# Kernel optimization log

Hardware: AMD Instinct MI355X
Metric: run time of the kernel (lower is better)

## Reference

```python
import jax, jax.numpy as jnp
import numpy as np

NE, NR, D, H, L = 200000, 500, 128, 4, 2
HD = D // H
N, E, B = 32768, 262144, 256
MARGIN = 1.0


def setup_inputs() -> dict:
    key = jax.random.key(0)
    ks = jax.random.split(key, 16)
    nrm = lambda k, shp, s=0.05: jax.random.normal(k, shp, jnp.float32) * s
    inp = {
        'ent_emb': nrm(ks[0], (NE, D)),
        'rel_emb': nrm(ks[1], (NR, D)),
        'rel_prior': nrm(ks[2], (NR, 1)),
    }
    for i, nm in enumerate(['Wq', 'Wk', 'Wv', 'Wo', 'Wek', 'Wev']):
        inp[nm] = nrm(ks[3 + i], (L, D, D))
    for gi, g in enumerate(['h', 't', 'n']):
        kb = jax.random.fold_in(key, 100 + gi)
        k1, k2, k3, k4 = jax.random.split(kb, 4)
        inp[f'x_{g}'] = jax.random.randint(k1, (N,), 0, NE, jnp.int32)
        inp[f'ei_{g}'] = jax.random.randint(k2, (2, E), 0, N, jnp.int32)
        inp[f'ea_{g}'] = jax.random.randint(k3, (E,), 0, NR, jnp.int32)
        inp[f'y_{g}'] = jax.random.randint(k4, (B,), 0, N // B, jnp.int32)
        inp[f's_{g}'] = jnp.full((B,), N // B, dtype=jnp.int32)
    inp['sample'] = jax.random.randint(ks[9], (B, 3), 0, NR, jnp.int32)
    return inp


def gnn_embed(ent_emb, rel_emb, rel_prior, Wq, Wk, Wv, Wo, Wek, Wev, x, ei, ea, y, s):
    n = x.shape[0]
    h = ent_emb[x]                    # [N, D] node features (embedding lookup)
    e_emb = rel_emb[ea]               # [E, D] edge relation embedding
    e_pri = rel_prior[ea]             # [E, 1] scalar relation prior gate
    src, dst = ei[0], ei[1]
    scale = 1.0 / np.sqrt(HD).astype(np.float32)
    for l in range(L):
        q = (h @ Wq[l]).reshape(n, H, HD)[dst]                               # [E,H,HD]
        k = (h @ Wk[l]).reshape(n, H, HD)[src] + (e_emb @ Wek[l]).reshape(-1, H, HD)
        v = (h @ Wv[l]).reshape(n, H, HD)[src] + (e_emb @ Wev[l]).reshape(-1, H, HD)
        score = jnp.sum(q * k, axis=-1) * scale * e_pri                      # [E,H]
        # segment softmax over incoming edges of each destination node
        m = jax.ops.segment_max(score, dst, num_segments=n)
        m = jnp.where(jnp.isfinite(m), m, 0.0)
        ex = jnp.exp(score - m[dst])
        den = jax.ops.segment_sum(ex, dst, num_segments=n)[dst]
        alpha = ex / (den + 1e-16)                                           # [E,H]
        msg = jax.ops.segment_sum((alpha[..., None] * v).reshape(-1, D), dst, num_segments=n)
        h = jax.nn.gelu(h + msg @ Wo[l])                                     # residual + activation
    # get_real_index: exclusive cumsum of graph sizes + local target index
    offsets = jnp.concatenate([jnp.zeros((1,), s.dtype), jnp.cumsum(s)[:-1]])
    return h[offsets + y]             # [B, D]


def reference(ent_emb, rel_emb, rel_prior, Wq, Wk, Wv, Wo, Wek, Wev,
              x_h, ei_h, ea_h, y_h, s_h,
              x_t, ei_t, ea_t, y_t, s_t,
              x_n, ei_n, ea_n, y_n, s_n, sample):
    g = lambda x, ei, ea, y, s: gnn_embed(ent_emb, rel_emb, rel_prior, Wq, Wk, Wv, Wo, Wek, Wev, x, ei, ea, y, s)
    h = g(x_h, ei_h, ea_h, y_h, s_h)[:, None, :]   # [B,1,D]
    t = g(x_t, ei_t, ea_t, y_t, s_t)[:, None, :]
    tn = g(x_n, ei_n, ea_n, y_n, s_n)[:, None, :]
    r = rel_emb[sample[:, 1]][:, None, :]          # [B,1,D]
    proj_t = h + r                                 # TransE projection
    pos = jnp.linalg.norm(t - proj_t + 1e-8, axis=2)   # [B,1]
    negs = jnp.linalg.norm(t - tn + 1e-8, axis=2)      # [B,1]
    neg = jnp.mean(negs, axis=-1)                      # [B]
    # MarginRankingLoss(pos, neg, target=-1): mean(max(0, (pos-neg)+margin)); broadcasts [B,1]-[B] -> [B,B]
    loss = jnp.mean(jnp.maximum(pos - neg + MARGIN, 0.0))
    return loss
```

## Files before the change

### kernel.cpp

```cpp
#include <hip/hip_runtime.h>
#include <hip/hip_bf16.h>
#include <math.h>

#define NEC 200000
#define NRC 500
#define DD 128
#define LLC 2
#define NNODE 32768
#define EEDGE 262144
#define BBATCH 256
#define NG 3
#define BCAP 32
#define NSB 32
#define EPG (EEDGE / NSB)
#define CNTW (NNODE / 4)

typedef __attribute__((ext_vector_type(8))) short short8;
typedef __attribute__((ext_vector_type(4))) float floatx4;
typedef __attribute__((ext_vector_type(2))) float floatx2;

__device__ __forceinline__ float bf2f(unsigned short u) {
  union { unsigned int i; float f; } c; c.i = ((unsigned int)u) << 16; return c.f;
}
__device__ __forceinline__ unsigned short f2bf(float f) {
  union { float f; unsigned int i; } c; c.f = f;
  unsigned int x = c.i;
  unsigned int r = x + 0x7fffu + ((x >> 16) & 1u);
  return (unsigned short)(r >> 16);
}
__device__ __forceinline__ float bfu_lo(unsigned int u) {
  union { unsigned int i; float f; } c; c.i = u << 16; return c.f;
}
__device__ __forceinline__ float bfu_hi(unsigned int u) {
  union { unsigned int i; float f; } c; c.i = u & 0xffff0000u; return c.f;
}

__device__ __forceinline__ bool detect_fm(const void* ent) {
  unsigned int u = ((const unsigned int*)ent)[threadIdx.x & 63];
  bool big = fabsf(bfu_lo(u)) > 100.f;
  return __ballot(big) != 0ull;
}

__global__ __launch_bounds__(128) void k_prep(const void* ent, const void* rel,
    const void* prior, const void* Wq, const void* Wk, const void* Wv, const void* Wo,
    const void* Wek, const void* Wev,
    float* pris, unsigned short* WT, unsigned short* relk, unsigned short* relv) {
  bool fm = detect_fm(ent);
  int bid = blockIdx.x, tid = threadIdx.x;
  if (bid < 4) {
    int r = bid * 128 + tid;
    if (r < NRC) {
      float p = fm ? ((const float*)prior)[r] : bf2f(((const unsigned short*)prior)[r]);
      pris[r] = p * 0.17677669529663687f;
    }
  } else if (bid < 1028) {
    int t = (bid - 4) * 128 + tid;
    int mat = t >> 15;
    int rem = t & 32767;
    int l = rem >> 14;
    int p = rem & 16383;
    int d = p >> 7, c = p & 127;
    const void* W = mat == 0 ? Wq : (mat == 1 ? Wk : (mat == 2 ? Wv : Wo));
    size_t src = (size_t)l * DD * DD + (size_t)c * DD + d;
    float v = fm ? ((const float*)W)[src] : bf2f(((const unsigned short*)W)[src]);
    WT[(((size_t)mat * LLC + l) * DD + d) * DD + c] = f2bf(v);
  } else {
    int rid = bid - 1028;
    int which = rid / 1000;
    int l = (rid / 500) % 2;
    int r = rid % 500;
    int d = tid;
    size_t wofs = (size_t)l * DD * DD;
    const float* Wf = (const float*)(which ? Wev : Wek) + wofs;
    const unsigned short* Wb = (const unsigned short*)(which ? Wev : Wek) + wofs;
    __shared__ float re[DD];
    re[d] = fm ? ((const float*)rel)[r * DD + d] : bf2f(((const unsigned short*)rel)[r * DD + d]);
    __syncthreads();
    float acc = 0.f;
    if (fm) { for (int c = 0; c < DD; ++c) acc += re[c] * Wf[c * DD + d]; }
    else    { for (int c = 0; c < DD; ++c) acc += re[c] * bf2f(Wb[c * DD + d]); }
    unsigned short* out = which ? relv : relk;
    out[((size_t)l * NRC + r) * DD + d] = f2bf(acc);
  }
}

__global__ __launch_bounds__(256) void k_gather(const void* ent,
    const int* x0, const int* x1, const int* x2, unsigned short* hbf) {
  bool fm = detect_fm(ent);
  int bid = blockIdx.x, tid = threadIdx.x;
  int rbase = bid * 64;
  int g = rbase >> 15;
  const int* x = g == 0 ? x0 : (g == 1 ? x1 : x2);
  int c = tid & 31;
  int j8 = tid >> 5;
  int rows[8], xs[8];
  #pragma unroll
  for (int k = 0; k < 8; ++k) {
    rows[k] = rbase + j8 + 8 * k;
    xs[k] = x[rows[k] & (NNODE - 1)];
  }
  if (fm) {
    float4 v[8];
    #pragma unroll
    for (int k = 0; k < 8; ++k)
      v[k] = *reinterpret_cast<const float4*>((const float*)ent + (size_t)xs[k] * DD + c * 4);
    #pragma unroll
    for (int k = 0; k < 8; ++k) {
      uint2 o;
      o.x = ((unsigned int)f2bf(v[k].y) << 16) | (unsigned int)f2bf(v[k].x);
      o.y = ((unsigned int)f2bf(v[k].w) << 16) | (unsigned int)f2bf(v[k].z);
      *reinterpret_cast<uint2*>(hbf + (size_t)rows[k] * DD + c * 4) = o;
    }
  } else {
    uint2 v[8];
    #pragma unroll
    for (int k = 0; k < 8; ++k)
      v[k] = *reinterpret_cast<const uint2*>((const unsigned short*)ent + (size_t)xs[k] * DD + c * 4);
    #pragma unroll
    for (int k = 0; k < 8; ++k)
      *reinterpret_cast<uint2*>(hbf + (size_t)rows[k] * DD + c * 4) = v[k];
  }
}

__global__ __launch_bounds__(1024) void k_count(const int* ei0, const int* ei1,
    const int* ei2, unsigned int* cntw) {
  __shared__ unsigned int cnt[CNTW];
  int bid = blockIdx.x, tid = threadIdx.x;
  int g = bid / NSB, grp = bid % NSB;
  const int* ei = g == 0 ? ei0 : (g == 1 ? ei1 : ei2);
  #pragma unroll
  for (int i = 0; i < CNTW / 1024; ++i) cnt[i * 1024 + tid] = 0u;
  __syncthreads();
  int e0 = grp * EPG;
  #pragma unroll
  for (int i = 0; i < EPG / 1024; ++i) {
    int dst = ei[EEDGE + e0 + i * 1024 + tid];
    atomicAdd(&cnt[dst >> 2], 1u << ((dst & 3) * 8));
  }
  __syncthreads();
  unsigned int* out = cntw + (size_t)(g * NSB + grp) * CNTW;
  #pragma unroll
  for (int i = 0; i < CNTW / 1024; ++i) out[i * 1024 + tid] = cnt[i * 1024 + tid];
}

__global__ __launch_bounds__(256) void k_prefix(const unsigned int* cntw,
    unsigned int* basew, int* deg) {
  int flat = blockIdx.x * 256 + threadIdx.x;
  int g = flat / CNTW, wi = flat % CNTW;
  unsigned int r0 = 0, r1 = 0, r2 = 0, r3 = 0;
  for (int grp = 0; grp < NSB; ++grp) {
    size_t idx = (size_t)(g * NSB + grp) * CNTW + wi;
    unsigned int w = cntw[idx];
    basew[idx] = r0 | (r1 << 8) | (r2 << 16) | (r3 << 24);
    r0 += w & 255u; r1 += (w >> 8) & 255u; r2 += (w >> 16) & 255u; r3 += (w >> 24) & 255u;
  }
  int4 dv = {(int)r0, (int)r1, (int)r2, (int)r3};
  *reinterpret_cast<int4*>(deg + (size_t)g * NNODE + wi * 4) = dv;
}

__global__ __launch_bounds__(1024) void k_place(const int* ei0, const int* ei1,
    const int* ei2, const int* ea0, const int* ea1, const int* ea2,
    const unsigned int* basew, unsigned int* bucket) {
  __shared__ unsigned int cnt[CNTW];
  __shared__ unsigned int basel[CNTW];
  int bid = blockIdx.x, tid = threadIdx.x;
  int g = bid / NSB, grp = bid % NSB;
  const int* ei = g == 0 ? ei0 : (g == 1 ? ei1 : ei2);
  const int* ea = g == 0 ? ea0 : (g == 1 ? ea1 : ea2);
  const unsigned int* brow = basew + (size_t)(g * NSB + grp) * CNTW;
  #pragma unroll
  for (int i = 0; i < CNTW / 1024; ++i) {
    cnt[i * 1024 + tid] = 0u;
    basel[i * 1024 + tid] = brow[i * 1024 + tid];
  }
  __syncthreads();
  int e0 = grp * EPG;
  size_t gb = (size_t)g * NNODE;
  #pragma unroll
  for (int i = 0; i < EPG / 1024; ++i) {
    int e = e0 + i * 1024 + tid;
    int dst = ei[EEDGE + e];
    unsigned int src = (unsigned int)ei[e];
    unsigned int r = (unsigned int)ea[e];
    int sh = (dst & 3) * 8;
    unsigned int old = atomicAdd(&cnt[dst >> 2], 1u << sh);
    unsigned int lpos = (old >> sh) & 255u;
    unsigned int b = (basel[dst >> 2] >> sh) & 255u;
    unsigned int slot = b + lpos;
    if (slot < BCAP)
      bucket[(gb + dst) * BCAP + slot] = src | (r << 15);
  }
}

__device__ __forceinline__ void stage_wt(const unsigned short* WT, int tid,
                                         unsigned short (*Wt)[136]) {
  #pragma unroll
  for (int pass = 0; pass < 8; ++pass) {
    int idx = pass * 256 + tid;
    int d = idx >> 4, c0 = (idx & 15) << 3;
    *reinterpret_cast<short8*>(&Wt[d][c0]) =
        *reinterpret_cast<const short8*>(WT + d * DD + c0);
  }
}

__global__ __launch_bounds__(256) void k_gemm_qkv(const unsigned short* A,
    const unsigned short* WT, int layer, unsigned short* Qo, unsigned char* KV) {
  __shared__ unsigned short Wt[DD][136];
  int mat = blockIdx.y;
  int g = blockIdx.z;
  const unsigned short* Ag = A + (size_t)g * NNODE * DD;
  int tid = threadIdx.x;
  stage_wt(WT + ((size_t)mat * LLC + layer) * DD * DD, tid, Wt);
  __syncthreads();
  int w = tid >> 6, lane = tid & 63;
  int m = lane & 15, quad = lane >> 4;
  int row = blockIdx.x * 64 + w * 16 + m;
  floatx4 acc[8];
  #pragma unroll
  for (int t = 0; t < 8; ++t) acc[t] = (floatx4){0.f, 0.f, 0.f, 0.f};
  const unsigned short* arow = Ag + (size_t)row * DD;
  #pragma unroll
  for (int ks = 0; ks < 4; ++ks) {
    short8 a = *reinterpret_cast<const short8*>(arow + ks * 32 + quad * 8);
    #pragma unroll
    for (int t = 0; t < 8; ++t) {
      short8 b = *reinterpret_cast<const short8*>(&Wt[t * 16 + m][ks * 32 + quad * 8]);
      acc[t] = __builtin_amdgcn_mfma_f32_16x16x32_bf16(a, b, acc[t], 0, 0, 0);
    }
  }
  __syncthreads();
  unsigned short* ut = &Wt[0][0];
  #pragma unroll
  for (int t = 0; t < 8; ++t) {
    #pragma unroll
    for (int r = 0; r < 4; ++r) {
      ut[(w * 16 + quad * 4 + r) * 136 + t * 16 + m] = f2bf(acc[t][r]);
    }
  }
  __syncthreads();
  int rowbase = blockIdx.x * 64;
  if (mat == 0) {
    unsigned short* Og = Qo + (size_t)g * NNODE * DD;
    #pragma unroll
    for (int k = 0; k < 4; ++k) {
      int flat = k * 256 + tid;
      int rw = flat >> 4, c8 = flat & 15;
      short8 v = *reinterpret_cast<const short8*>(ut + rw * 136 + c8 * 8);
      *reinterpret_cast<short8*>(Og + (size_t)(rowbase + rw) * DD + c8 * 8) = v;
    }
  } else {
    unsigned char* kvb = KV + (size_t)g * NNODE * 256 + (mat == 1 ? 0 : 128);
    #pragma unroll
    for (int k = 0; k < 2; ++k) {
      int flat = k * 256 + tid;
      int rw = flat >> 3, c16 = flat & 7;
      const unsigned short* p = ut + rw * 136 + c16 * 16;
      uint4 a = *reinterpret_cast<const uint4*>(p);
      uint4 b = *reinterpret_cast<const uint4*>(p + 8);
      unsigned int w0 = __builtin_amdgcn_cvt_pk_fp8_f32(bfu_lo(a.x), bfu_hi(a.x), 0u, false);
      w0 = __builtin_amdgcn_cvt_pk_fp8_f32(bfu_lo(a.y), bfu_hi(a.y), w0, true);
      unsigned int w1 = __builtin_amdgcn_cvt_pk_fp8_f32(bfu_lo(a.z), bfu_hi(a.z), 0u, false);
      w1 = __builtin_amdgcn_cvt_pk_fp8_f32(bfu_lo(a.w), bfu_hi(a.w), w1, true);
      unsigned int w2 = __builtin_amdgcn_cvt_pk_fp8_f32(bfu_lo(b.x), bfu_hi(b.x), 0u, false);
      w2 = __builtin_amdgcn_cvt_pk_fp8_f32(bfu_lo(b.y), bfu_hi(b.y), w2, true);
      unsigned int w3 = __builtin_amdgcn_cvt_pk_fp8_f32(bfu_lo(b.z), bfu_hi(b.z), 0u, false);
      w3 = __builtin_amdgcn_cvt_pk_fp8_f32(bfu_lo(b.w), bfu_hi(b.w), w3, true);
      uint4 o = {w0, w1, w2, w3};
      *reinterpret_cast<uint4*>(kvb + (size_t)(rowbase + rw) * 256 + c16 * 16) = o;
    }
  }
}

__global__ __launch_bounds__(256) void k_gemm_o(const unsigned short* A,
    const unsigned short* WT, int layer, unsigned short* hbf) {
  __shared__ unsigned short Wt[DD][136];
  int g = blockIdx.y;
  const unsigned short* Ag = A + (size_t)g * NNODE * DD;
  unsigned short* hbg = hbf + (size_t)g * NNODE * DD;
  int tid = threadIdx.x;
  stage_wt(WT + ((size_t)3 * LLC + layer) * DD * DD, tid, Wt);
  __syncthreads();
  int w = tid >> 6, lane = tid & 63;
  int m = lane & 15, quad = lane >> 4;
  int row = blockIdx.x * 64 + w * 16 + m;
  floatx4 acc[8];
  #pragma unroll
  for (int t = 0; t < 8; ++t) acc[t] = (floatx4){0.f, 0.f, 0.f, 0.f};
  const unsigned short* arow = Ag + (size_t)row * DD;
  #pragma unroll
  for (int ks = 0; ks < 4; ++ks) {
    short8 a = *reinterpret_cast<const short8*>(arow + ks * 32 + quad * 8);
    #pragma unroll
    for (int t = 0; t < 8; ++t) {
      short8 b = *reinterpret_cast<const short8*>(&Wt[t * 16 + m][ks * 32 + quad * 8]);
      acc[t] = __builtin_amdgcn_mfma_f32_16x16x32_bf16(a, b, acc[t], 0, 0, 0);
    }
  }
  __syncthreads();
  float* ft = (float*)&Wt[0][0];
  #pragma unroll
  for (int t = 0; t < 8; ++t) {
    #pragma unroll
    for (int r = 0; r < 4; ++r) {
      ft[(w * 16 + quad * 4 + r) * 136 + t * 16 + m] = acc[t][r];
    }
  }
  __syncthreads();
  int rowbase = blockIdx.x * 64;
  #pragma unroll
  for (int k = 0; k < 8; ++k) {
    int flat = k * 256 + tid;
    int rw = flat >> 5, c4 = flat & 31;
    float4 v = *reinterpret_cast<const float4*>(ft + rw * 136 + c4 * 4);
    size_t gi = (size_t)(rowbase + rw) * DD + c4 * 4;
    uint2 hv = *reinterpret_cast<const uint2*>(hbg + gi);
    float h0 = bfu_lo(hv.x), h1 = bfu_hi(hv.x), h2 = bfu_lo(hv.y), h3 = bfu_hi(hv.y);
    float r0, r1, r2, r3;
    {
      float xv = v.x + h0;
      float z2 = 1.5957691216057308f * (xv + 0.044715f * xv * xv * xv);
      r0 = xv / (1.f + __expf(-z2));
      xv = v.y + h1;
      z2 = 1.5957691216057308f * (xv + 0.044715f * xv * xv * xv);
      r1 = xv / (1.f + __expf(-z2));
      xv = v.z + h2;
      z2 = 1.5957691216057308f * (xv + 0.044715f * xv * xv * xv);
      r2 = xv / (1.f + __expf(-z2));
      xv = v.w + h3;
      z2 = 1.5957691216057308f * (xv + 0.044715f * xv * xv * xv);
      r3 = xv / (1.f + __expf(-z2));
    }
    uint2 o;
    o.x = ((unsigned int)f2bf(r1) << 16) | (unsigned int)f2bf(r0);
    o.y = ((unsigned int)f2bf(r3) << 16) | (unsigned int)f2bf(r2);
    *reinterpret_cast<uint2*>(hbg + gi) = o;
  }
}

__global__ __launch_bounds__(256) void k_attn(const unsigned short* Q, const unsigned char* KV,
    const unsigned short* relk, const unsigned short* relv,
    const float* pris, const int* deg, const unsigned int* bucket, int layer,
    unsigned short* msgb) {
  int w = threadIdx.x >> 6, lane = threadIdx.x & 63;
  int half = lane >> 5;
  int hq = (lane >> 4) & 1;
  int sl = lane & 15;
  int g = blockIdx.y;
  int dst = blockIdx.x * 8 + w * 2 + half;
  const unsigned short* rk = relk + (size_t)layer * NRC * DD;
  const unsigned short* rv = relv + (size_t)layer * NRC * DD;
  const unsigned char* KVg = KV + (size_t)g * NNODE * 256;
  size_t gofs = (size_t)g * NNODE * DD;

  uint4 qu = *reinterpret_cast<const uint4*>(Q + gofs + (size_t)dst * DD + sl * 8);
  floatx2 q01 = {bfu_lo(qu.x), bfu_hi(qu.x)};
  floatx2 q23 = {bfu_lo(qu.y), bfu_hi(qu.y)};
  floatx2 q45 = {bfu_lo(qu.z), bfu_hi(qu.z)};
  floatx2 q67 = {bfu_lo(qu.w), bfu_hi(qu.w)};

  float den = 0.f;
  floatx2 m01 = {0.f, 0.f}, m23 = {0.f, 0.f}, m45 = {0.f, 0.f}, m67 = {0.f, 0.f};
  int dg = deg[g * NNODE + dst]; if (dg > BCAP) dg = BCAP;
  size_t base = ((size_t)g * NNODE + dst) * BCAP;
  if (dg > 0) {
    int niter = (dg + 1) >> 1;
    int e1 = 2 + hq; if (e1 >= dg) e1 = dg - 1;
    unsigned int pe_nxt = bucket[base + (hq < dg ? hq : dg - 1)];
    unsigned int pe_fut = bucket[base + e1];
    int src = (int)(pe_nxt & 32767u);
    int r = (int)(pe_nxt >> 15);
    const unsigned char* kvrow = KVg + (size_t)src * 256;
    uint2 k8 = *reinterpret_cast<const uint2*>(kvrow + sl * 8);
    uint2 v8 = *reinterpret_cast<const uint2*>(kvrow + 128 + sl * 8);
    uint4 rku = *reinterpret_cast<const uint4*>(rk + (size_t)r * DD + sl * 8);
    uint4 rvu = *reinterpret_cast<const uint4*>(rv + (size_t)r * DD + sl * 8);
    float p = pris[r];
    pe_nxt = pe_fut;
    for (int i = 0; i < niter; ++i) {
      int ef = 2 * (i + 2) + hq; if (ef >= dg) ef = dg - 1;
      pe_fut = bucket[base + ef];
      int nsrc = (int)(pe_nxt & 32767u);
      int nr = (int)(pe_nxt >> 15);
      const unsigned char* nkv = KVg + (size_t)nsrc * 256;
      uint2 nk8 = *reinterpret_cast<const uint2*>(nkv + sl * 8);
      uint2 nv8 = *reinterpret_cast<const uint2*>(nkv + 128 + sl * 8);
      uint4 nrku = *reinterpret_cast<const uint4*>(rk + (size_t)nr * DD + sl * 8);
      uint4 nrvu = *reinterpret_cast<const uint4*>(rv + (size_t)nr * DD + sl * 8);
      float np = pris[nr];
      floatx2 kk01 = __builtin_amdgcn_cvt_pk_f32_fp8(k8.x, false);
      floatx2 kk23 = __builtin_amdgcn_cvt_pk_f32_fp8(k8.x, true);
      floatx2 kk45 = __builtin_amdgcn_cvt_pk_f32_fp8(k8.y, false);
      floatx2 kk67 = __builtin_amdgcn_cvt_pk_f32_fp8(k8.y, true);
      floatx2 rk01 = {bfu_lo(rku.x), bfu_hi(rku.x)};
      floatx2 rk23 = {bfu_lo(rku.y), bfu_hi(rku.y)};
      floatx2 rk45 = {bfu_lo(rku.z), bfu_hi(rku.z)};
      floatx2 rk67 = {bfu_lo(rku.w), bfu_hi(rku.w)};
      floatx2 sv = (kk01 + rk01) * q01;
      sv += (kk23 + rk23) * q23;
      sv += (kk45 + rk45) * q45;
      sv += (kk67 + rk67) * q67;
      float s = sv.x + sv.y;
      s += __shfl_xor(s, 1); s += __shfl_xor(s, 2);
      bool valid = (2 * i + hq) < dg;
      float ex = valid ? __expf(s * p) : 0.f;
      floatx2 vv01 = __builtin_amdgcn_cvt_pk_f32_fp8(v8.x, false);
      floatx2 vv23 = __builtin_amdgcn_cvt_pk_f32_fp8(v8.x, true);
      floatx2 vv45 = __builtin_amdgcn_cvt_pk_f32_fp8(v8.y, false);
      floatx2 vv67 = __builtin_amdgcn_cvt_pk_f32_fp8(v8.y, true);
      floatx2 rv01 = {bfu_lo(rvu.x), bfu_hi(rvu.x)};
      floatx2 rv23 = {bfu_lo(rvu.y), bfu_hi(rvu.y)};
      floatx2 rv45 = {bfu_lo(rvu.z), bfu_hi(rvu.z)};
      floatx2 rv67 = {bfu_lo(rvu.w), bfu_hi(rvu.w)};
      floatx2 ex2 = {ex, ex};
      den += ex;
      m01 += ex2 * (vv01 + rv01);
      m23 += ex2 * (vv23 + rv23);
      m45 += ex2 * (vv45 + rv45);
      m67 += ex2 * (vv67 + rv67);
      k8 = nk8; v8 = nv8; rku = nrku; rvu = nrvu; p = np;
      pe_nxt = pe_fut;
    }
  }
  den += __shfl_xor(den, 16);
  m01.x += __shfl_xor(m01.x, 16);
  m01.y += __shfl_xor(m01.y, 16);
  m23.x += __shfl_xor(m23.x, 16);
  m23.y += __shfl_xor(m23.y, 16);
  m45.x += __shfl_xor(m45.x, 16);
  m45.y += __shfl_xor(m45.y, 16);
  m67.x += __shfl_xor(m67.x, 16);
  m67.y += __shfl_xor(m67.y, 16);
  float inv = 1.f / (den + 1e-16f);
  if (hq == 0) {
    uint4 o;
    o.x = ((unsigned int)f2bf(m01.y * inv) << 16) | (unsigned int)f2bf(m01.x * inv);
    o.y = ((unsigned int)f2bf(m23.y * inv) << 16) | (unsigned int)f2bf(m23.x * inv);
    o.z = ((unsigned int)f2bf(m45.y * inv) << 16) | (unsigned int)f2bf(m45.x * inv);
    o.w = ((unsigned int)f2bf(m67.y * inv) << 16) | (unsigned int)f2bf(m67.x * inv);
    *reinterpret_cast<uint4*>(msgb + gofs + (size_t)dst * DD + sl * 8) = o;
  }
}

__global__ __launch_bounds__(128) void k_ep(const unsigned short* hbf, const void* ent,
    const void* rel,
    const int* y0, const int* s0, const int* y1, const int* s1, const int* y2, const int* s2,
    const int* sample, float* pos, float* neg) {
  bool fm = detect_fm(ent);
  int b = blockIdx.x, d = threadIdx.x;
  int oh = 0, ot = 0, on = 0;
  for (int j = 0; j < b; ++j) { oh += s0[j]; ot += s1[j]; on += s2[j]; }
  int ih = oh + y0[b], it = ot + y1[b], in_ = on + y2[b];
  float th = bf2f(hbf[((size_t)0 * NNODE + ih) * DD + d]);
  float tt = bf2f(hbf[((size_t)1 * NNODE + it) * DD + d]);
  float tn = bf2f(hbf[((size_t)2 * NNODE + in_) * DD + d]);
  int r = sample[b * 3 + 1];
  float rr = fm ? ((const float*)rel)[r * DD + d] : bf2f(((const unsigned short*)rel)[r * DD + d]);
  float dp = tt - (th + rr) + 1e-8f;
  float dn = tt - tn + 1e-8f;
  float ap = dp * dp, an = dn * dn;
  for (int o = 32; o > 0; o >>= 1) { ap += __shfl_down(ap, o); an += __shfl_down(an, o); }
  __shared__ float sa[2], sb[2];
  if ((d & 63) == 0) { sa[d >> 6] = ap; sb[d >> 6] = an; }
  __syncthreads();
  if (d == 0) { pos[b] = sqrtf(sa[0] + sa[1]); neg[b] = sqrtf(sb[0] + sb[1]); }
}

__global__ __launch_bounds__(256) void k_hinge(const float* pos, const float* neg,
    const void* ent, void* out) {
  bool fm = detect_fm(ent);
  __shared__ float ns[BBATCH];
  __shared__ float wsum[4];
  int t = threadIdx.x;
  ns[t] = neg[t];
  float pb = pos[t];
  __syncthreads();
  float local = 0.f;
  for (int j = 0; j < BBATCH; ++j) {
    float v = pb - ns[j] + 1.0f;
    local += v > 0.f ? v : 0.f;
  }
  for (int o = 32; o > 0; o >>= 1) local += __shfl_down(local, o);
  if ((t & 63) == 0) wsum[t >> 6] = local;
  __syncthreads();
  if (t == 0) {
    float loss = (wsum[0] + wsum[1] + wsum[2] + wsum[3]) * (1.f / (256.f * 256.f));
    if (fm) ((float*)out)[0] = loss;
    else    ((unsigned short*)out)[0] = f2bf(loss);
  }
}

extern "C" void kernel_launch(void* const* d_in, const int* in_sizes, int n_in,
                              void* d_out, int out_size, void* d_ws, size_t ws_size,
                              hipStream_t stream) {
  const void* ent   = d_in[0];
  const void* rel   = d_in[1];
  const void* prior = d_in[2];
  const void* Wq  = d_in[3];
  const void* Wk  = d_in[4];
  const void* Wv  = d_in[5];
  const void* Wo  = d_in[6];
  const void* Wek = d_in[7];
  const void* Wev = d_in[8];
  const int* sample = (const int*)d_in[24];

  size_t off = 0;
  char* basep = (char*)d_ws;
  auto alloc = [&](size_t bytes) -> void* {
    void* r = basep + off;
    off = (off + bytes + 255) & ~(size_t)255;
    return r;
  };
  unsigned short* hbf  = (unsigned short*)alloc((size_t)NG * NNODE * DD * 2);
  unsigned short* Qb   = (unsigned short*)alloc((size_t)NG * NNODE * DD * 2);
  unsigned char*  KV   = (unsigned char*)alloc((size_t)NG * NNODE * 256);
  unsigned short* msgb = (unsigned short*)alloc((size_t)NG * NNODE * DD * 2);
  unsigned short* relk = (unsigned short*)alloc((size_t)LLC * NRC * DD * 2);
  unsigned short* relv = (unsigned short*)alloc((size_t)LLC * NRC * DD * 2);
  unsigned short* WT   = (unsigned short*)alloc((size_t)4 * LLC * DD * DD * 2);
  float* pris = (float*)alloc((size_t)NRC * 4);
  int*   deg  = (int*)alloc((size_t)NG * NNODE * 4);
  unsigned int* bucket = (unsigned int*)alloc((size_t)NG * NNODE * BCAP * 4);
  unsigned int* cntw   = (unsigned int*)alloc((size_t)NG * NSB * CNTW * 4);
  unsigned int* basew  = (unsigned int*)alloc((size_t)NG * NSB * CNTW * 4);
  float* pos  = (float*)alloc((size_t)BBATCH * 4);
  float* neg  = (float*)alloc((size_t)BBATCH * 4);

  const int* x0  = (const int*)d_in[9],  *x1 = (const int*)d_in[14], *x2 = (const int*)d_in[19];
  const int* ei0 = (const int*)d_in[10], *ei1 = (const int*)d_in[15], *ei2 = (const int*)d_in[20];
  const int* ea0 = (const int*)d_in[11], *ea1 = (const int*)d_in[16], *ea2 = (const int*)d_in[21];
  const int* y0  = (const int*)d_in[12], *y1 = (const int*)d_in[17], *y2 = (const int*)d_in[22];
  const int* s0  = (const int*)d_in[13], *s1 = (const int*)d_in[18], *s2 = (const int*)d_in[23];

  k_prep<<<3028, 128, 0, stream>>>(ent, rel, prior, Wq, Wk, Wv, Wo, Wek, Wev,
                                   pris, WT, relk, relv);
  k_gather<<<1536, 256, 0, stream>>>(ent, x0, x1, x2, hbf);
  k_count<<<NG * NSB, 1024, 0, stream>>>(ei0, ei1, ei2, cntw);
  k_prefix<<<NG * CNTW / 256, 256, 0, stream>>>(cntw, basew, deg);
  k_place<<<NG * NSB, 1024, 0, stream>>>(ei0, ei1, ei2, ea0, ea1, ea2, basew, bucket);
  for (int l = 0; l < LLC; ++l) {
    k_gemm_qkv<<<dim3(NNODE / 64, 3, NG), 256, 0, stream>>>(hbf, WT, l, Qb, KV);
    k_attn<<<dim3(NNODE / 8, NG), 256, 0, stream>>>(Qb, KV, relk, relv, pris, deg, bucket, l, msgb);
    k_gemm_o<<<dim3(NNODE / 64, NG), 256, 0, stream>>>(msgb, WT, l, hbf);
  }
  k_ep<<<BBATCH, 128, 0, stream>>>(hbf, ent, rel, y0, s0, y1, s1, y2, s2, sample, pos, neg);
  k_hinge<<<1, BBATCH, 0, stream>>>(pos, neg, ent, d_out);
}
```

Before: 452.0 us.

## Interleave K/V fp8 rows and fuse relation tables into fp32 interleaved layout

The K and V fp8 node tables are interleaved in 8-byte chunks, so each lane fetches its K and V slices with one 16-byte load instead of two 8-byte loads. The per-relation K and V projection tables are merged into one fp32 table with the same interleaving, which removes the bf16 unpacking in the attention loop. The V half of the relation row is loaded late, at the current iteration, to keep prefetch registers low. In exchange the relation table doubles in size and gives up bf16 rounding, and the late V load is exposed to latency.

```diff
diff --git a/kernel.cpp b/kernel.cpp
--- a/kernel.cpp
+++ b/kernel.cpp
@@ -44,7 +44,7 @@
 __global__ __launch_bounds__(128) void k_prep(const void* ent, const void* rel,
     const void* prior, const void* Wq, const void* Wk, const void* Wv, const void* Wo,
     const void* Wek, const void* Wev,
-    float* pris, unsigned short* WT, unsigned short* relk, unsigned short* relv) {
+    float* pris, unsigned short* WT, float* relkv) {
   bool fm = detect_fm(ent);
   int bid = blockIdx.x, tid = threadIdx.x;
   if (bid < 4) {
@@ -79,8 +79,7 @@
     float acc = 0.f;
     if (fm) { for (int c = 0; c < DD; ++c) acc += re[c] * Wf[c * DD + d]; }
     else    { for (int c = 0; c < DD; ++c) acc += re[c] * bf2f(Wb[c * DD + d]); }
-    unsigned short* out = which ? relv : relk;
-    out[((size_t)l * NRC + r) * DD + d] = f2bf(acc);
+    relkv[((size_t)l * NRC + r) * 256 + (d >> 3) * 16 + (d & 7) + (which ? 8 : 0)] = acc;
   }
 }
 
@@ -249,7 +248,7 @@
       *reinterpret_cast<short8*>(Og + (size_t)(rowbase + rw) * DD + c8 * 8) = v;
     }
   } else {
-    unsigned char* kvb = KV + (size_t)g * NNODE * 256 + (mat == 1 ? 0 : 128);
+    unsigned char* kvb = KV + (size_t)g * NNODE * 256 + (mat == 1 ? 0 : 8);
     #pragma unroll
     for (int k = 0; k < 2; ++k) {
       int flat = k * 256 + tid;
@@ -265,8 +264,10 @@
       w2 = __builtin_amdgcn_cvt_pk_fp8_f32(bfu_lo(b.y), bfu_hi(b.y), w2, true);
       unsigned int w3 = __builtin_amdgcn_cvt_pk_fp8_f32(bfu_lo(b.z), bfu_hi(b.z), 0u, false);
       w3 = __builtin_amdgcn_cvt_pk_fp8_f32(bfu_lo(b.w), bfu_hi(b.w), w3, true);
-      uint4 o = {w0, w1, w2, w3};
-      *reinterpret_cast<uint4*>(kvb + (size_t)(rowbase + rw) * 256 + c16 * 16) = o;
+      size_t rofs = (size_t)(rowbase + rw) * 256;
+      uint2 lo = {w0, w1}, hi = {w2, w3};
+      *reinterpret_cast<uint2*>(kvb + rofs + (2 * c16) * 16) = lo;
+      *reinterpret_cast<uint2*>(kvb + rofs + (2 * c16 + 1) * 16) = hi;
     }
   }
 }
@@ -338,17 +339,15 @@
 }
 
 __global__ __launch_bounds__(256) void k_attn(const unsigned short* Q, const unsigned char* KV,
-    const unsigned short* relk, const unsigned short* relv,
-    const float* pris, const int* deg, const unsigned int* bucket, int layer,
-    unsigned short* msgb) {
+    const float* relkv, const float* pris, const int* deg, const unsigned int* bucket,
+    int layer, unsigned short* msgb) {
   int w = threadIdx.x >> 6, lane = threadIdx.x & 63;
   int half = lane >> 5;
   int hq = (lane >> 4) & 1;
   int sl = lane & 15;
   int g = blockIdx.y;
   int dst = blockIdx.x * 8 + w * 2 + half;
-  const unsigned short* rk = relk + (size_t)layer * NRC * DD;
-  const unsigned short* rv = relv + (size_t)layer * NRC * DD;
+  const float* rtab = relkv + (size_t)layer * NRC * 256;
   const unsigned char* KVg = KV + (size_t)g * NNODE * 256;
   size_t gofs = (size_t)g * NNODE * DD;
 
@@ -369,55 +368,49 @@
     unsigned int pe_fut = bucket[base + e1];
     int src = (int)(pe_nxt & 32767u);
     int r = (int)(pe_nxt >> 15);
-    const unsigned char* kvrow = KVg + (size_t)src * 256;
-    uint2 k8 = *reinterpret_cast<const uint2*>(kvrow + sl * 8);
-    uint2 v8 = *reinterpret_cast<const uint2*>(kvrow + 128 + sl * 8);
-    uint4 rku = *reinterpret_cast<const uint4*>(rk + (size_t)r * DD + sl * 8);
-    uint4 rvu = *reinterpret_cast<const uint4*>(rv + (size_t)r * DD + sl * 8);
+    uint4 kv8 = *reinterpret_cast<const uint4*>(KVg + (size_t)src * 256 + sl * 16);
+    const float* rrow = rtab + r * 256 + sl * 16;
+    float4 ra = *reinterpret_cast<const float4*>(rrow);
+    float4 rb = *reinterpret_cast<const float4*>(rrow + 4);
     float p = pris[r];
+    int rcur = r;
     pe_nxt = pe_fut;
     for (int i = 0; i < niter; ++i) {
       int ef = 2 * (i + 2) + hq; if (ef >= dg) ef = dg - 1;
       pe_fut = bucket[base + ef];
       int nsrc = (int)(pe_nxt & 32767u);
       int nr = (int)(pe_nxt >> 15);
-      const unsigned char* nkv = KVg + (size_t)nsrc * 256;
-      uint2 nk8 = *reinterpret_cast<const uint2*>(nkv + sl * 8);
-      uint2 nv8 = *reinterpret_cast<const uint2*>(nkv + 128 + sl * 8);
-      uint4 nrku = *reinterpret_cast<const uint4*>(rk + (size_t)nr * DD + sl * 8);
-      uint4 nrvu = *reinterpret_cast<const uint4*>(rv + (size_t)nr * DD + sl * 8);
+      uint4 nkv = *reinterpret_cast<const uint4*>(KVg + (size_t)nsrc * 256 + sl * 16);
+      const float* nrrow = rtab + nr * 256 + sl * 16;
+      float4 nra = *reinterpret_cast<const float4*>(nrrow);
+      float4 nrb = *reinterpret_cast<const float4*>(nrrow + 4);
       float np = pris[nr];
-      floatx2 kk01 = __builtin_amdgcn_cvt_pk_f32_fp8(k8.x, false);
-      floatx2 kk23 = __builtin_amdgcn_cvt_pk_f32_fp8(k8.x, true);
-      floatx2 kk45 = __builtin_amdgcn_cvt_pk_f32_fp8(k8.y, false);
-      floatx2 kk67 = __builtin_amdgcn_cvt_pk_f32_fp8(k8.y, true);
-      floatx2 rk01 = {bfu_lo(rku.x), bfu_hi(rku.x)};
-      floatx2 rk23 = {bfu_lo(rku.y), bfu_hi(rku.y)};
-      floatx2 rk45 = {bfu_lo(rku.z), bfu_hi(rku.z)};
-      floatx2 rk67 = {bfu_lo(rku.w), bfu_hi(rku.w)};
-      floatx2 sv = (kk01 + rk01) * q01;
-      sv += (kk23 + rk23) * q23;
-      sv += (kk45 + rk45) * q45;
-      sv += (kk67 + rk67) * q67;
+      const float* crrow = rtab + rcur * 256 + sl * 16;
+      float4 rc = *reinterpret_cast<const float4*>(crrow + 8);
+      float4 rd = *reinterpret_cast<const float4*>(crrow + 12);
+      floatx2 kk01 = __builtin_amdgcn_cvt_pk_f32_fp8(kv8.x, false);
+      floatx2 kk23 = __builtin_amdgcn_cvt_pk_f32_fp8(kv8.x, true);
+      floatx2 kk45 = __builtin_amdgcn_cvt_pk_f32_fp8(kv8.y, false);
+      floatx2 kk67 = __builtin_amdgcn_cvt_pk_f32_fp8(kv8.y, true);
+      floatx2 sv = (kk01 + (floatx2){ra.x, ra.y}) * q01;
+      sv += (kk23 + (floatx2){ra.z, ra.w}) * q23;
+      sv += (kk45 + (floatx2){rb.x, rb.y}) * q45;
+      sv += (kk67 + (floatx2){rb.z, rb.w}) * q67;
       float s = sv.x + sv.y;
       s += __shfl_xor(s, 1); s += __shfl_xor(s, 2);
       bool valid = (2 * i + hq) < dg;
       float ex = valid ? __expf(s * p) : 0.f;
-      floatx2 vv01 = __builtin_amdgcn_cvt_pk_f32_fp8(v8.x, false);
-      floatx2 vv23 = __builtin_amdgcn_cvt_pk_f32_fp8(v8.x, true);
-      floatx2 vv45 = __builtin_amdgcn_cvt_pk_f32_fp8(v8.y, false);
-      floatx2 vv67 = __builtin_amdgcn_cvt_pk_f32_fp8(v8.y, true);
-      floatx2 rv01 = {bfu_lo(rvu.x), bfu_hi(rvu.x)};
-      floatx2 rv23 = {bfu_lo(rvu.y), bfu_hi(rvu.y)};
-      floatx2 rv45 = {bfu_lo(rvu.z), bfu_hi(rvu.z)};
-      floatx2 rv67 = {bfu_lo(rvu.w), bfu_hi(rvu.w)};
+      floatx2 vv01 = __builtin_amdgcn_cvt_pk_f32_fp8(kv8.z, false);
+      floatx2 vv23 = __builtin_amdgcn_cvt_pk_f32_fp8(kv8.z, true);
+      floatx2 vv45 = __builtin_amdgcn_cvt_pk_f32_fp8(kv8.w, false);
+      floatx2 vv67 = __builtin_amdgcn_cvt_pk_f32_fp8(kv8.w, true);
       floatx2 ex2 = {ex, ex};
       den += ex;
-      m01 += ex2 * (vv01 + rv01);
-      m23 += ex2 * (vv23 + rv23);
-      m45 += ex2 * (vv45 + rv45);
-      m67 += ex2 * (vv67 + rv67);
-      k8 = nk8; v8 = nv8; rku = nrku; rvu = nrvu; p = np;
+      m01 += ex2 * (vv01 + (floatx2){rc.x, rc.y});
+      m23 += ex2 * (vv23 + (floatx2){rc.z, rc.w});
+      m45 += ex2 * (vv45 + (floatx2){rd.x, rd.y});
+      m67 += ex2 * (vv67 + (floatx2){rd.z, rd.w});
+      kv8 = nkv; ra = nra; rb = nrb; p = np; rcur = nr;
       pe_nxt = pe_fut;
     }
   }
@@ -514,8 +507,7 @@
   unsigned short* Qb   = (unsigned short*)alloc((size_t)NG * NNODE * DD * 2);
   unsigned char*  KV   = (unsigned char*)alloc((size_t)NG * NNODE * 256);
   unsigned short* msgb = (unsigned short*)alloc((size_t)NG * NNODE * DD * 2);
-  unsigned short* relk = (unsigned short*)alloc((size_t)LLC * NRC * DD * 2);
-  unsigned short* relv = (unsigned short*)alloc((size_t)LLC * NRC * DD * 2);
+  float* relkv = (float*)alloc((size_t)LLC * NRC * 256 * 4);
   unsigned short* WT   = (unsigned short*)alloc((size_t)4 * LLC * DD * DD * 2);
   float* pris = (float*)alloc((size_t)NRC * 4);
   int*   deg  = (int*)alloc((size_t)NG * NNODE * 4);
@@ -532,14 +524,14 @@
   const int* s0  = (const int*)d_in[13], *s1 = (const int*)d_in[18], *s2 = (const int*)d_in[23];
 
   k_prep<<<3028, 128, 0, stream>>>(ent, rel, prior, Wq, Wk, Wv, Wo, Wek, Wev,
-                                   pris, WT, relk, relv);
+                                   pris, WT, relkv);
   k_gather<<<1536, 256, 0, stream>>>(ent, x0, x1, x2, hbf);
   k_count<<<NG * NSB, 1024, 0, stream>>>(ei0, ei1, ei2, cntw);
   k_prefix<<<NG * CNTW / 256, 256, 0, stream>>>(cntw, basew, deg);
   k_place<<<NG * NSB, 1024, 0, stream>>>(ei0, ei1, ei2, ea0, ea1, ea2, basew, bucket);
   for (int l = 0; l < LLC; ++l) {
     k_gemm_qkv<<<dim3(NNODE / 64, 3, NG), 256, 0, stream>>>(hbf, WT, l, Qb, KV);
-    k_attn<<<dim3(NNODE / 8, NG), 256, 0, stream>>>(Qb, KV, relk, relv, pris, deg, bucket, l, msgb);
+    k_attn<<<dim3(NNODE / 8, NG), 256, 0, stream>>>(Qb, KV, relkv, pris, deg, bucket, l, msgb);
     k_gemm_o<<<dim3(NNODE / 64, NG), 256, 0, stream>>>(msgb, WT, l, hbf);
   }
   k_ep<<<BBATCH, 128, 0, stream>>>(hbf, ent, rel, y0, s0, y1, s1, y2, s2, sample, pos, neg);
```

New measurement: 553.5 us. 22.5% more time.

## Reuse A tile across Q/K/V in one block; use full wave per destination

Applied to the files above, without the earlier changes.

The QKV GEMM now loads each block's activation rows into registers once and loops over the three weight matrices, restaging each weight into shared memory. This removes the triple read of the activations and shrinks the grid by a factor of three. The attention kernel now gives each destination node a full 64-lane wave with four edges in flight per iteration, where previously two destinations shared a wave. This raises memory-level parallelism per node, at the cost of extra cross-lane reductions and idle lanes for low-degree nodes.

```diff
diff --git a/kernel.cpp b/kernel.cpp
--- a/kernel.cpp
+++ b/kernel.cpp
@@ -206,67 +206,73 @@
 __global__ __launch_bounds__(256) void k_gemm_qkv(const unsigned short* A,
     const unsigned short* WT, int layer, unsigned short* Qo, unsigned char* KV) {
   __shared__ unsigned short Wt[DD][136];
-  int mat = blockIdx.y;
-  int g = blockIdx.z;
+  int g = blockIdx.y;
   const unsigned short* Ag = A + (size_t)g * NNODE * DD;
   int tid = threadIdx.x;
-  stage_wt(WT + ((size_t)mat * LLC + layer) * DD * DD, tid, Wt);
-  __syncthreads();
   int w = tid >> 6, lane = tid & 63;
   int m = lane & 15, quad = lane >> 4;
   int row = blockIdx.x * 64 + w * 16 + m;
-  floatx4 acc[8];
-  #pragma unroll
-  for (int t = 0; t < 8; ++t) acc[t] = (floatx4){0.f, 0.f, 0.f, 0.f};
+  int rowbase = blockIdx.x * 64;
   const unsigned short* arow = Ag + (size_t)row * DD;
-  #pragma unroll
-  for (int ks = 0; ks < 4; ++ks) {
-    short8 a = *reinterpret_cast<const short8*>(arow + ks * 32 + quad * 8);
+  short8 a[4];
+  #pragma unroll
+  for (int ks = 0; ks < 4; ++ks)
+    a[ks] = *reinterpret_cast<const short8*>(arow + ks * 32 + quad * 8);
+
+  for (int mat = 0; mat < 3; ++mat) {
+    if (mat) __syncthreads();
+    stage_wt(WT + ((size_t)mat * LLC + layer) * DD * DD, tid, Wt);
+    __syncthreads();
+    floatx4 acc[8];
+    #pragma unroll
+    for (int t = 0; t < 8; ++t) acc[t] = (floatx4){0.f, 0.f, 0.f, 0.f};
+    #pragma unroll
+    for (int ks = 0; ks < 4; ++ks) {
+      #pragma unroll
+      for (int t = 0; t < 8; ++t) {
+        short8 b = *reinterpret_cast<const short8*>(&Wt[t * 16 + m][ks * 32 + quad * 8]);
+        acc[t] = __builtin_amdgcn_mfma_f32_16x16x32_bf16(a[ks], b, acc[t], 0, 0, 0);
+      }
+    }
+    __syncthreads();
+    unsigned short* ut = &Wt[0][0];
     #pragma unroll
     for (int t = 0; t < 8; ++t) {
-      short8 b = *reinterpret_cast<const short8*>(&Wt[t * 16 + m][ks * 32 + quad * 8]);
-      acc[t] = __builtin_amdgcn_mfma_f32_16x16x32_bf16(a, b, acc[t], 0, 0, 0);
-    }
-  }
-  __syncthreads();
-  unsigned short* ut = &Wt[0][0];
-  #pragma unroll
-  for (int t = 0; t < 8; ++t) {
-    #pragma unroll
-    for (int r = 0; r < 4; ++r) {
-      ut[(w * 16 + quad * 4 + r) * 136 + t * 16 + m] = f2bf(acc[t][r]);
-    }
-  }
-  __syncthreads();
-  int rowbase = blockIdx.x * 64;
-  if (mat == 0) {
-    unsigned short* Og = Qo + (size_t)g * NNODE * DD;
-    #pragma unroll
-    for (int k = 0; k < 4; ++k) {
-      int flat = k * 256 + tid;
-      int rw = flat >> 4, c8 = flat & 15;
-      short8 v = *reinterpret_cast<const short8*>(ut + rw * 136 + c8 * 8);
-      *reinterpret_cast<short8*>(Og + (size_t)(rowbase + rw) * DD + c8 * 8) = v;
-    }
-  } else {
-    unsigned char* kvb = KV + (size_t)g * NNODE * 256 + (mat == 1 ? 0 : 128);
-    #pragma unroll
-    for (int k = 0; k < 2; ++k) {
-      int flat = k * 256 + tid;
-      int rw = flat >> 3, c16 = flat & 7;
-      const unsigned short* p = ut + rw * 136 + c16 * 16;
-      uint4 a = *reinterpret_cast<const uint4*>(p);
-      uint4 b = *reinterpret_cast<const uint4*>(p + 8);
-      unsigned int w0 = __builtin_amdgcn_cvt_pk_fp8_f32(bfu_lo(a.x), bfu_hi(a.x), 0u, false);
-      w0 = __builtin_amdgcn_cvt_pk_fp8_f32(bfu_lo(a.y), bfu_hi(a.y), w0, true);
-      unsigned int w1 = __builtin_amdgcn_cvt_pk_fp8_f32(bfu_lo(a.z), bfu_hi(a.z), 0u, false);
-      w1 = __builtin_amdgcn_cvt_pk_fp8_f32(bfu_lo(a.w), bfu_hi(a.w), w1, true);
-      unsigned int w2 = __builtin_amdgcn_cvt_pk_fp8_f32(bfu_lo(b.x), bfu_hi(b.x), 0u, false);
-      w2 = __builtin_amdgcn_cvt_pk_fp8_f32(bfu_lo(b.y), bfu_hi(b.y), w2, true);
-      unsigned int w3 = __builtin_amdgcn_cvt_pk_fp8_f32(bfu_lo(b.z), bfu_hi(b.z), 0u, false);
-      w3 = __builtin_amdgcn_cvt_pk_fp8_f32(bfu_lo(b.w), bfu_hi(b.w), w3, true);
-      uint4 o = {w0, w1, w2, w3};
-      *reinterpret_cast<uint4*>(kvb + (size_t)(rowbase + rw) * 256 + c16 * 16) = o;
+      #pragma unroll
+      for (int r = 0; r < 4; ++r) {
+        ut[(w * 16 + quad * 4 + r) * 136 + t * 16 + m] = f2bf(acc[t][r]);
+      }
+    }
+    __syncthreads();
+    if (mat == 0) {
+      unsigned short* Og = Qo + (size_t)g * NNODE * DD;
+      #pragma unroll
+      for (int k = 0; k < 4; ++k) {
+        int flat = k * 256 + tid;
+        int rw = flat >> 4, c8 = flat & 15;
+        short8 v = *reinterpret_cast<const short8*>(ut + rw * 136 + c8 * 8);
+        *reinterpret_cast<short8*>(Og + (size_t)(rowbase + rw) * DD + c8 * 8) = v;
+      }
+    } else {
+      unsigned char* kvb = KV + (size_t)g * NNODE * 256 + (mat == 1 ? 0 : 128);
+      #pragma unroll
+      for (int k = 0; k < 2; ++k) {
+        int flat = k * 256 + tid;
+        int rw = flat >> 3, c16 = flat & 7;
+        const unsigned short* p = ut + rw * 136 + c16 * 16;
+        uint4 va = *reinterpret_cast<const uint4*>(p);
+        uint4 vb = *reinterpret_cast<const uint4*>(p + 8);
+        unsigned int w0 = __builtin_amdgcn_cvt_pk_fp8_f32(bfu_lo(va.x), bfu_hi(va.x), 0u, false);
+        w0 = __builtin_amdgcn_cvt_pk_fp8_f32(bfu_lo(va.y), bfu_hi(va.y), w0, true);
+        unsigned int w1 = __builtin_amdgcn_cvt_pk_fp8_f32(bfu_lo(va.z), bfu_hi(va.z), 0u, false);
+        w1 = __builtin_amdgcn_cvt_pk_fp8_f32(bfu_lo(va.w), bfu_hi(va.w), w1, true);
+        unsigned int w2 = __builtin_amdgcn_cvt_pk_fp8_f32(bfu_lo(vb.x), bfu_hi(vb.x), 0u, false);
+        w2 = __builtin_amdgcn_cvt_pk_fp8_f32(bfu_lo(vb.y), bfu_hi(vb.y), w2, true);
+        unsigned int w3 = __builtin_amdgcn_cvt_pk_fp8_f32(bfu_lo(vb.z), bfu_hi(vb.z), 0u, false);
+        w3 = __builtin_amdgcn_cvt_pk_fp8_f32(bfu_lo(vb.w), bfu_hi(vb.w), w3, true);
+        uint4 o = {w0, w1, w2, w3};
+        *reinterpret_cast<uint4*>(kvb + (size_t)(rowbase + rw) * 256 + c16 * 16) = o;
+      }
     }
   }
 }
@@ -342,11 +348,10 @@
     const float* pris, const int* deg, const unsigned int* bucket, int layer,
     unsigned short* msgb) {
   int w = threadIdx.x >> 6, lane = threadIdx.x & 63;
-  int half = lane >> 5;
-  int hq = (lane >> 4) & 1;
+  int sq = lane >> 4;
   int sl = lane & 15;
   int g = blockIdx.y;
-  int dst = blockIdx.x * 8 + w * 2 + half;
+  int dst = blockIdx.x * 4 + w;
   const unsigned short* rk = relk + (size_t)layer * NRC * DD;
   const unsigned short* rv = relv + (size_t)layer * NRC * DD;
   const unsigned char* KVg = KV + (size_t)g * NNODE * 256;
@@ -363,9 +368,9 @@
   int dg = deg[g * NNODE + dst]; if (dg > BCAP) dg = BCAP;
   size_t base = ((size_t)g * NNODE + dst) * BCAP;
   if (dg > 0) {
-    int niter = (dg + 1) >> 1;
-    int e1 = 2 + hq; if (e1 >= dg) e1 = dg - 1;
-    unsigned int pe_nxt = bucket[base + (hq < dg ? hq : dg - 1)];
+    int niter = (dg + 3) >> 2;
+    int e1 = 4 + sq; if (e1 >= dg) e1 = dg - 1;
+    unsigned int pe_nxt = bucket[base + (sq < dg ? sq : dg - 1)];
     unsigned int pe_fut = bucket[base + e1];
     int src = (int)(pe_nxt & 32767u);
     int r = (int)(pe_nxt >> 15);
@@ -377,7 +382,7 @@
     float p = pris[r];
     pe_nxt = pe_fut;
     for (int i = 0; i < niter; ++i) {
-      int ef = 2 * (i + 2) + hq; if (ef >= dg) ef = dg - 1;
+      int ef = 4 * (i + 2) + sq; if (ef >= dg) ef = dg - 1;
       pe_fut = bucket[base + ef];
       int nsrc = (int)(pe_nxt & 32767u);
       int nr = (int)(pe_nxt >> 15);
@@ -401,7 +406,7 @@
       sv += (kk67 + rk67) * q67;
       float s = sv.x + sv.y;
       s += __shfl_xor(s, 1); s += __shfl_xor(s, 2);
-      bool valid = (2 * i + hq) < dg;
+      bool valid = (4 * i + sq) < dg;
       float ex = valid ? __expf(s * p) : 0.f;
       floatx2 vv01 = __builtin_amdgcn_cvt_pk_f32_fp8(v8.x, false);
       floatx2 vv23 = __builtin_amdgcn_cvt_pk_f32_fp8(v8.x, true);
@@ -421,17 +426,17 @@
       pe_nxt = pe_fut;
     }
   }
-  den += __shfl_xor(den, 16);
-  m01.x += __shfl_xor(m01.x, 16);
-  m01.y += __shfl_xor(m01.y, 16);
-  m23.x += __shfl_xor(m23.x, 16);
-  m23.y += __shfl_xor(m23.y, 16);
-  m45.x += __shfl_xor(m45.x, 16);
-  m45.y += __shfl_xor(m45.y, 16);
-  m67.x += __shfl_xor(m67.x, 16);
-  m67.y += __shfl_xor(m67.y, 16);
+  den += __shfl_xor(den, 16); den += __shfl_xor(den, 32);
+  m01.x += __shfl_xor(m01.x, 16); m01.x += __shfl_xor(m01.x, 32);
+  m01.y += __shfl_xor(m01.y, 16); m01.y += __shfl_xor(m01.y, 32);
+  m23.x += __shfl_xor(m23.x, 16); m23.x += __shfl_xor(m23.x, 32);
+  m23.y += __shfl_xor(m23.y, 16); m23.y += __shfl_xor(m23.y, 32);
+  m45.x += __shfl_xor(m45.x, 16); m45.x += __shfl_xor(m45.x, 32);
+  m45.y += __shfl_xor(m45.y, 16); m45.y += __shfl_xor(m45.y, 32);
+  m67.x += __shfl_xor(m67.x, 16); m67.x += __shfl_xor(m67.x, 32);
+  m67.y += __shfl_xor(m67.y, 16); m67.y += __shfl_xor(m67.y, 32);
   float inv = 1.f / (den + 1e-16f);
-  if (hq == 0) {
+  if (sq == 0) {
     uint4 o;
     o.x = ((unsigned int)f2bf(m01.y * inv) << 16) | (unsigned int)f2bf(m01.x * inv);
     o.y = ((unsigned int)f2bf(m23.y * inv) << 16) | (unsigned int)f2bf(m23.x * inv);
@@ -538,8 +543,8 @@
   k_prefix<<<NG * CNTW / 256, 256, 0, stream>>>(cntw, basew, deg);
   k_place<<<NG * NSB, 1024, 0, stream>>>(ei0, ei1, ei2, ea0, ea1, ea2, basew, bucket);
   for (int l = 0; l < LLC; ++l) {
-    k_gemm_qkv<<<dim3(NNODE / 64, 3, NG), 256, 0, stream>>>(hbf, WT, l, Qb, KV);
-    k_attn<<<dim3(NNODE / 8, NG), 256, 0, stream>>>(Qb, KV, relk, relv, pris, deg, bucket, l, msgb);
+    k_gemm_qkv<<<dim3(NNODE / 64, NG), 256, 0, stream>>>(hbf, WT, l, Qb, KV);
+    k_attn<<<dim3(NNODE / 4, NG), 256, 0, stream>>>(Qb, KV, relk, relv, pris, deg, bucket, l, msgb);
     k_gemm_o<<<dim3(NNODE / 64, NG), 256, 0, stream>>>(msgb, WT, l, hbf);
   }
   k_ep<<<BBATCH, 128, 0, stream>>>(hbf, ent, rel, y0, s0, y1, s1, y2, s2, sample, pos, neg);
```

Result: slower. 471.2 us (+4.3%).
